# Performance work log

Hardware: AMD Instinct MI355X
Metric: run time of the kernel (lower is better)

Reference implementation:

```python
import jax, jax.numpy as jnp
import numpy as np

B, T, I, H = 256, 256, 2048, 128

def setup_inputs() -> dict:
    key = jax.random.key(0)
    ks = jax.random.split(key, 7)
    s = 1.0 / np.sqrt(H)  # torch RNN/Linear init scale
    return {
        "x": jax.random.normal(ks[0], (B, T, I), dtype=jnp.float32),
        "W_ih": jax.random.uniform(ks[1], (H, I), jnp.float32, -s, s),
        "W_hh": jax.random.uniform(ks[2], (H, H), jnp.float32, -s, s),
        "b_ih": jax.random.uniform(ks[3], (H,), jnp.float32, -s, s),
        "b_hh": jax.random.uniform(ks[4], (H,), jnp.float32, -s, s),
        "W_fc": jax.random.uniform(ks[5], (1, H), jnp.float32, -s, s),
        "b_fc": jax.random.uniform(ks[6], (1,), jnp.float32, -s, s),
    }

def reference(x, W_ih, W_hh, b_ih, b_hh, W_fc, b_fc):
    # Precompute input projection for all timesteps as one big GEMM: [B,T,H]
    xp = jnp.einsum('bti,hi->bth', x, W_ih) + (b_ih + b_hh)
    h0 = jnp.zeros((x.shape[0], W_hh.shape[0]), dtype=x.dtype)

    def step(h, xt):  # xt: [B,H]
        h = jnp.tanh(xt + h @ W_hh.T)
        return h, None

    hT, _ = jax.lax.scan(step, h0, jnp.swapaxes(xp, 0, 1))  # final hidden [B,H]
    out = hT @ W_fc.T + b_fc  # [B,1]
    return out.squeeze(1)     # [B]
```

## Files before the change

kernel.cpp:

```cpp
#include <hip/hip_runtime.h>
#include <hip/hip_bf16.h>
#include <math.h>

#define B_ 256
#define T_ 256
#define I_ 2048
#define H_ 128

typedef __attribute__((ext_vector_type(8))) short bf16x8;
typedef __attribute__((ext_vector_type(4))) float f32x4;

static __device__ inline short f2bf(float f) {
    __hip_bfloat16 h = __float2bfloat16(f);
    return *reinterpret_cast<short*>(&h);
}

#define BM 128
#define BK 32
#define LDSROW 40
#define NKT (I_ / BK)

__global__ __launch_bounds__(256, 2) void proj_mfma(
    const float* __restrict__ x, const float* __restrict__ Wih,
    const float* __restrict__ bih, const float* __restrict__ bhh,
    float* __restrict__ xp)
{
    __shared__ __align__(16) short As[2][BM * LDSROW];
    __shared__ __align__(16) short Bs[2][H_ * LDSROW];

    const int tid  = threadIdx.x;
    const int lane = tid & 63;
    const int wid  = tid >> 6;
    const int wr   = wid >> 1;
    const int wc   = wid & 1;
    const long row0 = (long)blockIdx.x * BM;

    const int srow = tid >> 3;
    const int skc  = tid & 7;

    const float* pA = x   + (row0 + srow) * I_ + skc * 4;
    const float* pB = Wih + (long)srow * I_ + skc * 4;
    const int ldsOff = srow * LDSROW + skc * 4;

    f32x4 acc[4][4];
    #pragma unroll
    for (int m = 0; m < 4; ++m)
        #pragma unroll
        for (int n = 0; n < 4; ++n)
            acc[m][n] = (f32x4){0.f, 0.f, 0.f, 0.f};

    float4 ra[4], rb[4];
    #pragma unroll
    for (int it = 0; it < 4; ++it) {
        ra[it] = *reinterpret_cast<const float4*>(pA + (long)it * 32 * I_);
        rb[it] = *reinterpret_cast<const float4*>(pB + (long)it * 32 * I_);
    }
    #pragma unroll
    for (int it = 0; it < 4; ++it) {
        short4 a4, b4;
        a4.x = f2bf(ra[it].x); a4.y = f2bf(ra[it].y);
        a4.z = f2bf(ra[it].z); a4.w = f2bf(ra[it].w);
        b4.x = f2bf(rb[it].x); b4.y = f2bf(rb[it].y);
        b4.z = f2bf(rb[it].z); b4.w = f2bf(rb[it].w);
        *reinterpret_cast<short4*>(&As[0][ldsOff + it * 32 * LDSROW]) = a4;
        *reinterpret_cast<short4*>(&Bs[0][ldsOff + it * 32 * LDSROW]) = b4;
    }
    #pragma unroll
    for (int it = 0; it < 4; ++it) {
        ra[it] = *reinterpret_cast<const float4*>(pA + (long)it * 32 * I_ + BK);
        rb[it] = *reinterpret_cast<const float4*>(pB + (long)it * 32 * I_ + BK);
    }
    __syncthreads();

    const int fr = lane & 15;
    const int fq = lane >> 4;
    const int aBase = (wr * 64 + fr) * LDSROW + fq * 8;
    const int bBase = (wc * 64 + fr) * LDSROW + fq * 8;

    int p = 0;
    for (int t = 0; t < NKT; ++t) {
        if (t + 1 < NKT) {
            #pragma unroll
            for (int it = 0; it < 4; ++it) {
                short4 a4, b4;
                a4.x = f2bf(ra[it].x); a4.y = f2bf(ra[it].y);
                a4.z = f2bf(ra[it].z); a4.w = f2bf(ra[it].w);
                b4.x = f2bf(rb[it].x); b4.y = f2bf(rb[it].y);
                b4.z = f2bf(rb[it].z); b4.w = f2bf(rb[it].w);
                *reinterpret_cast<short4*>(&As[p ^ 1][ldsOff + it * 32 * LDSROW]) = a4;
                *reinterpret_cast<short4*>(&Bs[p ^ 1][ldsOff + it * 32 * LDSROW]) = b4;
            }
        }
        if (t + 2 < NKT) {
            #pragma unroll
            for (int it = 0; it < 4; ++it) {
                ra[it] = *reinterpret_cast<const float4*>(
                    pA + (long)it * 32 * I_ + (t + 2) * BK);
                rb[it] = *reinterpret_cast<const float4*>(
                    pB + (long)it * 32 * I_ + (t + 2) * BK);
            }
        }
        bf16x8 af[4], bfr[4];
        #pragma unroll
        for (int f = 0; f < 4; ++f) {
            af[f]  = *reinterpret_cast<const bf16x8*>(&As[p][aBase + f * 16 * LDSROW]);
            bfr[f] = *reinterpret_cast<const bf16x8*>(&Bs[p][bBase + f * 16 * LDSROW]);
        }
        #pragma unroll
        for (int m = 0; m < 4; ++m)
            #pragma unroll
            for (int n = 0; n < 4; ++n)
                acc[m][n] = __builtin_amdgcn_mfma_f32_16x16x32_bf16(
                    af[m], bfr[n], acc[m][n], 0, 0, 0);
        __syncthreads();
        p ^= 1;
    }

    #pragma unroll
    for (int n = 0; n < 4; ++n) {
        const int col = wc * 64 + n * 16 + fr;
        const float bn = bih[col] + bhh[col];
        #pragma unroll
        for (int m = 0; m < 4; ++m) {
            const long rbase = row0 + wr * 64 + m * 16 + fq * 4;
            #pragma unroll
            for (int j = 0; j < 4; ++j)
                xp[(rbase + j) * H_ + col] = acc[m][n][j] + bn;
        }
    }
}

__global__ __launch_bounds__(256) void scan_kernel(
    const float* __restrict__ xp, const float* __restrict__ Whh,
    const float* __restrict__ Wfc, const float* __restrict__ bfc,
    float* __restrict__ out)
{
    __shared__ __align__(16) float hbuf[2][H_];

    const int tid  = threadIdx.x;
    const int lane = tid & 63;
    const int w    = tid >> 6;
    const int j    = w * 32 + (lane & 31);
    const int g    = lane >> 5;
    const int b    = blockIdx.x;

    float Wreg[64];
    {
        const float4* wp = reinterpret_cast<const float4*>(&Whh[(long)j * H_ + g * 64]);
        #pragma unroll
        for (int q = 0; q < 16; ++q) {
            const float4 wv = wp[q];
            Wreg[4*q]   = wv.x; Wreg[4*q+1] = wv.y;
            Wreg[4*q+2] = wv.z; Wreg[4*q+3] = wv.w;
        }
    }
    if (tid < H_) hbuf[0][tid] = 0.f;

    const float* xprow = xp + (long)b * T_ * H_ + j;
    float xa = xprow[0 * H_];
    float xb = xprow[1 * H_];
    float xc = xprow[2 * H_];
    float xd = xprow[3 * H_];
    __syncthreads();

    auto body = [&](int t, float xpv) {
        const float4* h4 = reinterpret_cast<const float4*>(&hbuf[t & 1][g * 64]);
        float a0 = 0.f, a1 = 0.f, a2 = 0.f, a3 = 0.f;
        #pragma unroll
        for (int q = 0; q < 16; ++q) {
            const float4 hh = h4[q];
            a0 += hh.x * Wreg[4*q];
            a1 += hh.y * Wreg[4*q+1];
            a2 += hh.z * Wreg[4*q+2];
            a3 += hh.w * Wreg[4*q+3];
        }
        float part = (a0 + a1) + (a2 + a3);
        part += __shfl_xor(part, 32);
        const float pre = part + xpv;
        const float e = __expf(2.f * pre);
        hbuf[(t + 1) & 1][j] = 1.f - 2.f / (e + 1.f);
        __syncthreads();
    };

    for (int t = 0; t < T_; t += 4) {
        float xu;
        xu = xa; if (t + 4 < T_) xa = xprow[(long)(t + 4) * H_];
        body(t + 0, xu);
        xu = xb; if (t + 5 < T_) xb = xprow[(long)(t + 5) * H_];
        body(t + 1, xu);
        xu = xc; if (t + 6 < T_) xc = xprow[(long)(t + 6) * H_];
        body(t + 2, xu);
        xu = xd; if (t + 7 < T_) xd = xprow[(long)(t + 7) * H_];
        body(t + 3, xu);
    }

    if (w == 0) {
        float v = hbuf[0][lane] * Wfc[lane] + hbuf[0][lane + 64] * Wfc[lane + 64];
        #pragma unroll
        for (int off = 32; off > 0; off >>= 1) v += __shfl_down(v, off);
        if (lane == 0) out[b] = v + bfc[0];
    }
}

extern "C" void kernel_launch(void* const* d_in, const int* in_sizes, int n_in,
                              void* d_out, int out_size, void* d_ws, size_t ws_size,
                              hipStream_t stream)
{
    const float* x   = (const float*)d_in[0];
    const float* Wih = (const float*)d_in[1];
    const float* Whh = (const float*)d_in[2];
    const float* bih = (const float*)d_in[3];
    const float* bhh = (const float*)d_in[4];
    const float* Wfc = (const float*)d_in[5];
    const float* bfc = (const float*)d_in[6];
    float* out = (float*)d_out;
    float* xp  = (float*)d_ws;

    proj_mfma<<<dim3((B_ * T_) / BM), dim3(256), 0, stream>>>(x, Wih, bih, bhh, xp);
    scan_kernel<<<dim3(B_), dim3(256), 0, stream>>>(xp, Whh, Wfc, bfc, out);
}
```

Baseline: 270.4 us.

## Load GEMM tiles directly into LDS with global_load_lds and XOR swizzle

Replaces the register-staged global-to-LDS path (load float4, convert to bf16, write LDS) with direct global_load_lds DMA of fp32 tiles into an XOR-swizzled LDS layout. The bf16 conversion moves to after the LDS read, just before the MFMA. The aim is to cut VGPR pressure and VALU/LDS-write work in the staging path and to hide global latency asynchronously. In exchange, LDS use doubles because it holds fp32, conversion is repeated per fragment read, and the prefetch distance drops from two tiles to one.

Result: no change. 271.1 us (+0.2%).

```diff
diff --git a/kernel.cpp b/kernel.cpp
--- a/kernel.cpp
+++ b/kernel.cpp
@@ -7,6 +7,10 @@
 #define I_ 2048
 #define H_ 128
 
+#define BM 128
+#define BK 32
+#define NKT (I_ / BK)
+
 typedef __attribute__((ext_vector_type(8))) short bf16x8;
 typedef __attribute__((ext_vector_type(4))) float f32x4;
 
@@ -15,18 +19,20 @@
     return *reinterpret_cast<short*>(&h);
 }
 
-#define BM 128
-#define BK 32
-#define LDSROW 40
-#define NKT (I_ / BK)
+static __device__ inline bf16x8 pack8(float4 a, float4 b) {
+    bf16x8 r;
+    r[0] = f2bf(a.x); r[1] = f2bf(a.y); r[2] = f2bf(a.z); r[3] = f2bf(a.w);
+    r[4] = f2bf(b.x); r[5] = f2bf(b.y); r[6] = f2bf(b.z); r[7] = f2bf(b.w);
+    return r;
+}
 
 __global__ __launch_bounds__(256, 2) void proj_mfma(
     const float* __restrict__ x, const float* __restrict__ Wih,
     const float* __restrict__ bih, const float* __restrict__ bhh,
     float* __restrict__ xp)
 {
-    __shared__ __align__(16) short As[2][BM * LDSROW];
-    __shared__ __align__(16) short Bs[2][H_ * LDSROW];
+    __shared__ __align__(16) float As[2][BM * BK];
+    __shared__ __align__(16) float Bs[2][H_ * BK];
 
     const int tid  = threadIdx.x;
     const int lane = tid & 63;
@@ -35,12 +41,8 @@
     const int wc   = wid & 1;
     const long row0 = (long)blockIdx.x * BM;
 
-    const int srow = tid >> 3;
-    const int skc  = tid & 7;
-
-    const float* pA = x   + (row0 + srow) * I_ + skc * 4;
-    const float* pB = Wih + (long)srow * I_ + skc * 4;
-    const int ldsOff = srow * LDSROW + skc * 4;
+    const int srow  = lane >> 3;
+    const int sunit = (lane & 7) ^ srow;
 
     f32x4 acc[4][4];
     #pragma unroll
@@ -49,62 +51,57 @@
         for (int n = 0; n < 4; ++n)
             acc[m][n] = (f32x4){0.f, 0.f, 0.f, 0.f};
 
-    float4 ra[4], rb[4];
-    #pragma unroll
-    for (int it = 0; it < 4; ++it) {
-        ra[it] = *reinterpret_cast<const float4*>(pA + (long)it * 32 * I_);
-        rb[it] = *reinterpret_cast<const float4*>(pB + (long)it * 32 * I_);
-    }
-    #pragma unroll
-    for (int it = 0; it < 4; ++it) {
-        short4 a4, b4;
-        a4.x = f2bf(ra[it].x); a4.y = f2bf(ra[it].y);
-        a4.z = f2bf(ra[it].z); a4.w = f2bf(ra[it].w);
-        b4.x = f2bf(rb[it].x); b4.y = f2bf(rb[it].y);
-        b4.z = f2bf(rb[it].z); b4.w = f2bf(rb[it].w);
-        *reinterpret_cast<short4*>(&As[0][ldsOff + it * 32 * LDSROW]) = a4;
-        *reinterpret_cast<short4*>(&Bs[0][ldsOff + it * 32 * LDSROW]) = b4;
-    }
-    #pragma unroll
-    for (int it = 0; it < 4; ++it) {
-        ra[it] = *reinterpret_cast<const float4*>(pA + (long)it * 32 * I_ + BK);
-        rb[it] = *reinterpret_cast<const float4*>(pB + (long)it * 32 * I_ + BK);
-    }
-    __syncthreads();
-
     const int fr = lane & 15;
     const int fq = lane >> 4;
-    const int aBase = (wr * 64 + fr) * LDSROW + fq * 8;
-    const int bBase = (wc * 64 + fr) * LDSROW + fq * 8;
+
+    const int rb0 = wid * 32;
+
+    #pragma unroll
+    for (int i = 0; i < 4; ++i) {
+        const int rbase = rb0 + i * 8;
+        const float* ga = x   + (row0 + rbase + srow) * I_ + sunit * 4;
+        const float* gb = Wih + (long)(rbase + srow) * I_ + sunit * 4;
+        __builtin_amdgcn_global_load_lds(
+            (const __attribute__((address_space(1))) void*)ga,
+            (__attribute__((address_space(3))) void*)&As[0][rbase * BK], 16, 0, 0);
+        __builtin_amdgcn_global_load_lds(
+            (const __attribute__((address_space(1))) void*)gb,
+            (__attribute__((address_space(3))) void*)&Bs[0][rbase * BK], 16, 0, 0);
+    }
+    __syncthreads();
 
     int p = 0;
     for (int t = 0; t < NKT; ++t) {
         if (t + 1 < NKT) {
+            const int kk = (t + 1) * BK;
             #pragma unroll
-            for (int it = 0; it < 4; ++it) {
-                short4 a4, b4;
-                a4.x = f2bf(ra[it].x); a4.y = f2bf(ra[it].y);
-                a4.z = f2bf(ra[it].z); a4.w = f2bf(ra[it].w);
-                b4.x = f2bf(rb[it].x); b4.y = f2bf(rb[it].y);
-                b4.z = f2bf(rb[it].z); b4.w = f2bf(rb[it].w);
-                *reinterpret_cast<short4*>(&As[p ^ 1][ldsOff + it * 32 * LDSROW]) = a4;
-                *reinterpret_cast<short4*>(&Bs[p ^ 1][ldsOff + it * 32 * LDSROW]) = b4;
+            for (int i = 0; i < 4; ++i) {
+                const int rbase = rb0 + i * 8;
+                const float* ga = x   + (row0 + rbase + srow) * I_ + kk + sunit * 4;
+                const float* gb = Wih + (long)(rbase + srow) * I_ + kk + sunit * 4;
+                __builtin_amdgcn_global_load_lds(
+                    (const __attribute__((address_space(1))) void*)ga,
+                    (__attribute__((address_space(3))) void*)&As[p ^ 1][rbase * BK], 16, 0, 0);
+                __builtin_amdgcn_global_load_lds(
+                    (const __attribute__((address_space(1))) void*)gb,
+                    (__attribute__((address_space(3))) void*)&Bs[p ^ 1][rbase * BK], 16, 0, 0);
             }
         }
-        if (t + 2 < NKT) {
-            #pragma unroll
-            for (int it = 0; it < 4; ++it) {
-                ra[it] = *reinterpret_cast<const float4*>(
-                    pA + (long)it * 32 * I_ + (t + 2) * BK);
-                rb[it] = *reinterpret_cast<const float4*>(
-                    pB + (long)it * 32 * I_ + (t + 2) * BK);
-            }
-        }
         bf16x8 af[4], bfr[4];
         #pragma unroll
         for (int f = 0; f < 4; ++f) {
-            af[f]  = *reinterpret_cast<const bf16x8*>(&As[p][aBase + f * 16 * LDSROW]);
-            bfr[f] = *reinterpret_cast<const bf16x8*>(&Bs[p][bBase + f * 16 * LDSROW]);
+            const int ra_ = wr * 64 + f * 16 + fr;
+            const float4 a0 = *reinterpret_cast<const float4*>(
+                &As[p][ra_ * BK + (((fq * 2)     ^ (ra_ & 7)) * 4)]);
+            const float4 a1 = *reinterpret_cast<const float4*>(
+                &As[p][ra_ * BK + (((fq * 2 + 1) ^ (ra_ & 7)) * 4)]);
+            af[f] = pack8(a0, a1);
+            const int rb_ = wc * 64 + f * 16 + fr;
+            const float4 b0 = *reinterpret_cast<const float4*>(
+                &Bs[p][rb_ * BK + (((fq * 2)     ^ (rb_ & 7)) * 4)]);
+            const float4 b1 = *reinterpret_cast<const float4*>(
+                &Bs[p][rb_ * BK + (((fq * 2 + 1) ^ (rb_ & 7)) * 4)]);
+            bfr[f] = pack8(b0, b1);
         }
         #pragma unroll
         for (int m = 0; m < 4; ++m)
```
